# Performance work log

Hardware: AMD Instinct MI355X
Metric: run time of the kernel (lower is better)

Reference implementation:

```python
import jax, jax.numpy as jnp
import numpy as np

NUM_CLASSES = 30522


def setup_inputs() -> dict:
    key = jax.random.key(0)
    k1, k2 = jax.random.split(key)
    B, S = 1024, 256
    input_ids = jax.random.randint(k1, (B, S), 0, NUM_CLASSES)  # token ids
    weights = jax.random.uniform(k2, (B, S, 1), dtype=jnp.float32)  # per-token weights
    return {"input_ids": input_ids, "weights": weights}


def reference(input_ids, weights):
    # Torch: one_hot(ids, V) * weights -> (B,S,V), max over dim=1 -> (B,V), cast bf16.
    # Equivalent (without the huge (B,S,V) intermediate): scatter-max of the
    # per-token weight into its vocab slot, with a 0 baseline everywhere
    # (non-matching one-hot entries contribute 0 to the max).
    B, S = input_ids.shape
    w = weights[..., 0]  # (B, S)
    base = jnp.zeros((B, NUM_CLASSES), dtype=weights.dtype)
    b_idx = jnp.arange(B)[:, None]  # (B, 1) broadcasts against (B, S) ids
    out = base.at[b_idx, input_ids].max(w)  # (B, V) scatter-max
    return out.astype(jnp.bfloat16)
```

## Files before the change

kernel.cpp:

```cpp
#include <hip/hip_runtime.h>
#include <cstdio>

#define BATCH     1024
#define SEQ       256
#define VOCAB     30522
#define ROW_U2    (VOCAB / 2)

extern "C" __global__ __launch_bounds__(256)
void TargetEncoder_532575944857_kernel(const int* __restrict__ ids,
                                       const float* __restrict__ ws,
                                       float* __restrict__ out) {
    __shared__ int   s_id[SEQ];
    __shared__ float s_w[SEQ];
    const int b = blockIdx.x, t = threadIdx.x;
    const int   id = ids[b * SEQ + t];
    const float w  = ws[b * SEQ + t];
    s_id[t] = id; s_w[t] = w;

    uint2* zrow = (uint2*)(out + (long long)b * VOCAB);
    const uint2 z = make_uint2(0u, 0u);
    for (int i = t; i < ROW_U2; i += SEQ) zrow[i] = z;

    __syncthreads();

    bool winner = ((unsigned)id < (unsigned)VOCAB);
    for (int j = 0; j < SEQ; ++j) {
        const int   oid = s_id[j];
        const float ow  = s_w[j];
        if (oid == id && (ow > w || (ow == w && j < t))) winner = false;
    }

    if (winner) {
        const unsigned u = __float_as_uint(w);
        const unsigned bits = ((u + 0x7FFFu + ((u >> 16) & 1u)) >> 16) << 16;
        out[(long long)b * VOCAB + id] = __uint_as_float(bits);
    }
}

extern "C" void kernel_launch(void* const* d_in, const int* in_sizes, int n_in,
                              void* d_out, int out_size, void* d_ws, size_t ws_size,
                              hipStream_t stream) {
    const int*   ids = (const int*)d_in[0];
    const float* ws  = (const float*)d_in[1];
    float*       out = (float*)d_out;

    TargetEncoder_532575944857_kernel<<<BATCH, SEQ, 0, stream>>>(ids, ws, out);

    hipStreamCaptureStatus cap = hipStreamCaptureStatusNone;
    (void)hipStreamIsCapturing(stream, &cap);
    if (cap == hipStreamCaptureStatusNone) {
        fprintf(stderr, "[TE r11] f32-output kernel launched (out_size=%d)\n",
                out_size);
        fflush(stderr);
    }
}
```

Measured before the change: 146.9 us.

## Replace in-block winner search with memset plus per-token atomicMax scatter

After: 136.7 us. 7.0% less time.

```diff
diff --git a/kernel.cpp b/kernel.cpp
--- a/kernel.cpp
+++ b/kernel.cpp
@@ -1,40 +1,26 @@
 #include <hip/hip_runtime.h>
-#include <cstdio>
 
-#define BATCH     1024
-#define SEQ       256
-#define VOCAB     30522
-#define ROW_U2    (VOCAB / 2)
+#define VOCAB 30522
+#define SEQ   256
 
 extern "C" __global__ __launch_bounds__(256)
 void TargetEncoder_532575944857_kernel(const int* __restrict__ ids,
                                        const float* __restrict__ ws,
-                                       float* __restrict__ out) {
-    __shared__ int   s_id[SEQ];
-    __shared__ float s_w[SEQ];
-    const int b = blockIdx.x, t = threadIdx.x;
-    const int   id = ids[b * SEQ + t];
-    const float w  = ws[b * SEQ + t];
-    s_id[t] = id; s_w[t] = w;
+                                       unsigned int* __restrict__ out,
+                                       int n_tok) {
+    const int t = blockIdx.x * blockDim.x + threadIdx.x;
+    if (t >= n_tok) return;
 
-    uint2* zrow = (uint2*)(out + (long long)b * VOCAB);
-    const uint2 z = make_uint2(0u, 0u);
-    for (int i = t; i < ROW_U2; i += SEQ) zrow[i] = z;
+    const int   id = ids[t];
+    const float w  = ws[t];
+    if ((unsigned)id >= (unsigned)VOCAB) return;
 
-    __syncthreads();
+    const unsigned u   = __float_as_uint(w);
+    const unsigned val = ((u + 0x7FFFu + ((u >> 16) & 1u)) >> 16) << 16;
+    if (val == 0u) return;
 
-    bool winner = ((unsigned)id < (unsigned)VOCAB);
-    for (int j = 0; j < SEQ; ++j) {
-        const int   oid = s_id[j];
-        const float ow  = s_w[j];
-        if (oid == id && (ow > w || (ow == w && j < t))) winner = false;
-    }
-
-    if (winner) {
-        const unsigned u = __float_as_uint(w);
-        const unsigned bits = ((u + 0x7FFFu + ((u >> 16) & 1u)) >> 16) << 16;
-        out[(long long)b * VOCAB + id] = __uint_as_float(bits);
-    }
+    const int b = t >> 8;
+    atomicMax(out + ((long long)b * VOCAB + id), val);
 }
 
 extern "C" void kernel_launch(void* const* d_in, const int* in_sizes, int n_in,
@@ -42,15 +28,10 @@
                               hipStream_t stream) {
     const int*   ids = (const int*)d_in[0];
     const float* ws  = (const float*)d_in[1];
-    float*       out = (float*)d_out;
+    const int n_tok  = in_sizes[0];
 
-    TargetEncoder_532575944857_kernel<<<BATCH, SEQ, 0, stream>>>(ids, ws, out);
+    (void)hipMemsetAsync(d_out, 0, (size_t)out_size * sizeof(float), stream);
 
-    hipStreamCaptureStatus cap = hipStreamCaptureStatusNone;
-    (void)hipStreamIsCapturing(stream, &cap);
-    if (cap == hipStreamCaptureStatusNone) {
-        fprintf(stderr, "[TE r11] f32-output kernel launched (out_size=%d)\n",
-                out_size);
-        fflush(stderr);
-    }
+    TargetEncoder_532575944857_kernel<<<(n_tok + 255) / 256, 256, 0, stream>>>(
+        ids, ws, (unsigned int*)d_out, n_tok);
 }
```
